# Kernel optimization log

Hardware: AMD Instinct MI355X
Metric: run time of the kernel (lower is better)

The kernel has to match this reference:

```python
import jax, jax.numpy as jnp
import numpy as np

B, U = 64, 512            # batch, max_units
AE = 1024
UE = 256                  # unit_embedding_size
A = 256                   # target_head_attention_size


def setup_inputs() -> dict:
    key = jax.random.key(0)
    ks = jax.random.split(key, 10)
    return {
        "autoregressive_embedding": jax.random.normal(ks[0], (B, U, AE), jnp.float32),
        "own_unit_embeddings": jax.random.normal(ks[1], (B, U, UE), jnp.float32),
        "enemy_unit_embeddings": jax.random.normal(ks[2], (B, U, UE), jnp.float32),
        "nr_own_units": jax.random.randint(ks[3], (B, 1), 0, U).astype(jnp.int64),
        "nr_units_enemy": jax.random.randint(ks[4], (B, 1), 0, U).astype(jnp.int64),
        "nr_own_flags": jax.random.randint(ks[5], (B, 1), 0, 8).astype(jnp.int64),
        "Wq": jax.random.normal(ks[6], (UE + AE, A), jnp.float32) * (1.0 / np.sqrt(UE + AE)),
        "bq": jnp.zeros((A,), jnp.float32),
        "Wk": jax.random.normal(ks[7], (UE, A), jnp.float32) * (1.0 / np.sqrt(UE)),
        "bk": jnp.zeros((A,), jnp.float32),
    }


def reference(autoregressive_embedding, own_unit_embeddings, enemy_unit_embeddings,
              nr_own_units, nr_units_enemy, nr_own_flags, Wq, bq, Wk, bk):
    # combined: [B, U, AE+UE]
    combined = jnp.concatenate([autoregressive_embedding, own_unit_embeddings], axis=2)
    queries = combined @ Wq + bq                       # [B, U, A]
    keys = enemy_unit_embeddings @ Wk + bk             # [B, U, A]
    attention = jnp.einsum("bqd,bkd->bqk", queries, keys) / (A ** 0.5)  # [B, U, U]
    # Vectorized mask: rows in [nr_own_flags, nr_own_units), cols in [0, nr_units_enemy)
    idx = jnp.arange(U)
    row_ok = (idx[None, :] >= nr_own_flags) & (idx[None, :] < nr_own_units)  # [B, U]
    col_ok = idx[None, :] < nr_units_enemy                                   # [B, U]
    mask = jnp.where(row_ok[:, :, None] & col_ok[:, None, :], 1.0, 1e-9)     # [B, U, U]
    return jax.nn.softmax(attention * mask, axis=-1)
```

## Files before the change

### kernel.cpp

```cpp
#include <hip/hip_runtime.h>

constexpr int B  = 64;
constexpr int U  = 512;
constexpr int AE = 1024;
constexpr int UE = 256;
constexpr int A  = 256;
constexpr int KQ = AE + UE;

typedef _Float16 f16x8 __attribute__((ext_vector_type(8)));
typedef float    f32x4 __attribute__((ext_vector_type(4)));

__global__ void prep(const float* __restrict__ Wq, const float* __restrict__ Wk,
                     _Float16* __restrict__ WqT, _Float16* __restrict__ WkT) {
    int idx = blockIdx.x * 256 + threadIdx.x;
    if (idx < KQ * A) {
        int k = idx >> 8, n = idx & 255;
        WqT[(size_t)n * KQ + k] = (_Float16)Wq[idx];
    } else {
        int j = idx - KQ * A;
        if (j < A * A) {
            int k = j >> 8, n = j & 255;
            WkT[(size_t)n * A + k] = (_Float16)Wk[j];
        }
    }
}

__global__ __launch_bounds__(256, 4) void gemm(
    const float* __restrict__ A1, int s1, int split,
    const float* __restrict__ A2, int s2,
    const _Float16* __restrict__ BT,
    const float* __restrict__ bias,
    _Float16* __restrict__ Out,
    int Ktot)
{
    __shared__ __align__(16) _Float16 Al[2][64][32];
    __shared__ __align__(16) _Float16 Bl[2][128][32];

    const int t    = threadIdx.x;
    const int lane = t & 63;
    const int w    = t >> 6;
    const int lm   = lane & 15;
    const int mbase = (blockIdx.x >> 1) * 64;
    const int nbase = (blockIdx.x & 1) * 128;

    const int wm  = (w & 1) * 32;
    const int wnl = (w >> 1) * 64;

    f32x4 acc[2][4] = {};

    const int ar = t & 63;
    const int kh = t >> 6;
    const int ap = kh >> 1;
    const size_t garow = mbase + ar;

    const int br = t >> 1;
    const int bs = t & 1;
    const size_t gbrow = nbase + br;

    float4 aR[4];
    f16x8  bR[4];

    auto loadA = [&](int k0) {
        int kg = k0 + kh * 16;
        const float* src = (kg < split) ? (A1 + garow * (size_t)s1 + kg)
                                        : (A2 + garow * (size_t)s2 + (kg - split));
        aR[0] = ((const float4*)src)[0];
        aR[1] = ((const float4*)src)[1];
        aR[2] = ((const float4*)src)[2];
        aR[3] = ((const float4*)src)[3];
    };
    auto loadB = [&](int k0) {
        const _Float16* src = BT + gbrow * (size_t)Ktot + k0 + bs * 32;
        bR[0] = ((const f16x8*)src)[0];
        bR[1] = ((const f16x8*)src)[1];
        bR[2] = ((const f16x8*)src)[2];
        bR[3] = ((const f16x8*)src)[3];
    };

    loadA(0);
    loadB(0);

    const int rsw = (lm >> 1) & 3;
    const int nk = Ktot >> 6;
    for (int kb = 0; kb < nk; kb++) {
        __syncthreads();
        {
            #pragma unroll
            for (int j = 0; j < 2; j++) {
                const float4 x = aR[j * 2], y = aR[j * 2 + 1];
                f16x8 hv;
                hv[0] = (_Float16)x.x; hv[1] = (_Float16)x.y;
                hv[2] = (_Float16)x.z; hv[3] = (_Float16)x.w;
                hv[4] = (_Float16)y.x; hv[5] = (_Float16)y.y;
                hv[6] = (_Float16)y.z; hv[7] = (_Float16)y.w;
                int c = (kh & 1) * 2 + j;
                *(f16x8*)(&Al[ap][ar][(c ^ ((ar >> 1) & 3)) * 8]) = hv;
            }
            #pragma unroll
            for (int j = 0; j < 4; j++)
                *(f16x8*)(&Bl[bs][br][(j ^ ((br >> 1) & 3)) * 8]) = bR[j];
        }
        __syncthreads();
        if (kb + 1 < nk) { loadA(kb * 64 + 64); loadB(kb * 64 + 64); }
        #pragma unroll
        for (int p = 0; p < 2; p++) {
            f16x8 af[2], bf[4];
            #pragma unroll
            for (int mt = 0; mt < 2; mt++)
                af[mt] = *(const f16x8*)(&Al[p][wm + mt * 16 + lm][((lane >> 4) ^ rsw) * 8]);
            #pragma unroll
            for (int nt = 0; nt < 4; nt++)
                bf[nt] = *(const f16x8*)(&Bl[p][wnl + nt * 16 + lm][((lane >> 4) ^ rsw) * 8]);
            #pragma unroll
            for (int mt = 0; mt < 2; mt++)
                #pragma unroll
                for (int nt = 0; nt < 4; nt++)
                    acc[mt][nt] = __builtin_amdgcn_mfma_f32_16x16x32_f16(
                        af[mt], bf[nt], acc[mt][nt], 0, 0, 0);
        }
    }

    const int rsub = (lane >> 4) * 4;
    #pragma unroll
    for (int nt = 0; nt < 4; nt++) {
        const int col = nbase + wnl + nt * 16 + lm;
        const float bv = bias[col];
        const int c5 = col >> 5, c31 = col & 31;
        #pragma unroll
        for (int mt = 0; mt < 2; mt++)
            #pragma unroll
            for (int r = 0; r < 4; r++) {
                int row = mbase + wm + mt * 16 + rsub + r;
                int bb = row >> 9, u = row & 511;
                Out[(((size_t)bb * 8 + c5) * 512 + u) * 32 + c31] =
                    (_Float16)(acc[mt][nt][r] + bv);
            }
    }
}

__global__ __launch_bounds__(256, 4) void attn(
    const _Float16* __restrict__ Qh, const _Float16* __restrict__ Kh,
    const int* __restrict__ nr_own_units, const int* __restrict__ nr_units_enemy,
    const int* __restrict__ nr_own_flags, float* __restrict__ Out)
{
    __shared__ float red[32][4];

    const int t    = threadIdx.x;
    const int lane = t & 63;
    const int w    = t >> 6;
    const int lm   = lane & 15;
    const int lk   = (lane >> 4) * 8;
    const int b    = blockIdx.y;
    const int qbase = blockIdx.x * 32;
    const int wn   = w * 128;

    const int nf = nr_own_flags[b];
    const int nu = nr_own_units[b];
    const int ne = nr_units_enemy[b];

    const _Float16* Qb = Qh + (size_t)b * 8 * 512 * 32;
    const _Float16* Kb = Kh + (size_t)b * 8 * 512 * 32;

    f32x4 acc[2][8] = {};

    #pragma unroll 2
    for (int c = 0; c < 8; c++) {
        f16x8 qf[2], bf[8];
        #pragma unroll
        for (int mt = 0; mt < 2; mt++)
            qf[mt] = *(const f16x8*)(Qb + ((size_t)c * 512 + qbase + mt * 16 + lm) * 32 + lk);
        #pragma unroll
        for (int nt = 0; nt < 8; nt++)
            bf[nt] = *(const f16x8*)(Kb + ((size_t)c * 512 + wn + nt * 16 + lm) * 32 + lk);
        #pragma unroll
        for (int mt = 0; mt < 2; mt++)
            #pragma unroll
            for (int nt = 0; nt < 8; nt++)
                acc[mt][nt] = __builtin_amdgcn_mfma_f32_16x16x32_f16(
                    qf[mt], bf[nt], acc[mt][nt], 0, 0, 0);
    }

    const int rsub = (lane >> 4) * 4;
    #pragma unroll
    for (int mt = 0; mt < 2; mt++)
        #pragma unroll
        for (int nt = 0; nt < 8; nt++)
            #pragma unroll
            for (int r = 0; r < 4; r++) {
                int uq = qbase + mt * 16 + rsub + r;
                int col = wn + nt * 16 + lm;
                bool ok = (col < ne) && (uq >= nf) && (uq < nu);
                acc[mt][nt][r] = acc[mt][nt][r] * 0.0625f * (ok ? 1.0f : 1e-9f);
            }

    float mx[2][4];
    #pragma unroll
    for (int mt = 0; mt < 2; mt++)
        #pragma unroll
        for (int r = 0; r < 4; r++) {
            float m = acc[mt][0][r];
            #pragma unroll
            for (int nt = 1; nt < 8; nt++) m = fmaxf(m, acc[mt][nt][r]);
            #pragma unroll
            for (int off = 1; off <= 8; off <<= 1) m = fmaxf(m, __shfl_xor(m, off));
            mx[mt][r] = m;
        }
    if (lm == 0) {
        #pragma unroll
        for (int mt = 0; mt < 2; mt++)
            #pragma unroll
            for (int r = 0; r < 4; r++)
                red[mt * 16 + rsub + r][w] = mx[mt][r];
    }
    __syncthreads();
    #pragma unroll
    for (int mt = 0; mt < 2; mt++)
        #pragma unroll
        for (int r = 0; r < 4; r++) {
            f32x4 v = *(const f32x4*)(&red[mt * 16 + rsub + r][0]);
            mx[mt][r] = fmaxf(fmaxf(v[0], v[1]), fmaxf(v[2], v[3]));
        }
    __syncthreads();

    float sm[2][4];
    #pragma unroll
    for (int mt = 0; mt < 2; mt++)
        #pragma unroll
        for (int r = 0; r < 4; r++) {
            float s = 0.f;
            #pragma unroll
            for (int nt = 0; nt < 8; nt++) {
                float e = __expf(acc[mt][nt][r] - mx[mt][r]);
                acc[mt][nt][r] = e;
                s += e;
            }
            #pragma unroll
            for (int off = 1; off <= 8; off <<= 1) s += __shfl_xor(s, off);
            sm[mt][r] = s;
        }
    if (lm == 0) {
        #pragma unroll
        for (int mt = 0; mt < 2; mt++)
            #pragma unroll
            for (int r = 0; r < 4; r++)
                red[mt * 16 + rsub + r][w] = sm[mt][r];
    }
    __syncthreads();

    #pragma unroll
    for (int mt = 0; mt < 2; mt++)
        #pragma unroll
        for (int r = 0; r < 4; r++) {
            int rl = mt * 16 + rsub + r;
            f32x4 v = *(const f32x4*)(&red[rl][0]);
            float inv = 1.0f / (v[0] + v[1] + v[2] + v[3]);
            float* orow = Out + ((size_t)b * 512 + qbase + rl) * 512 + wn + lm;
            #pragma unroll
            for (int nt = 0; nt < 8; nt++)
                orow[nt * 16] = acc[mt][nt][r] * inv;
        }
}

extern "C" void kernel_launch(void* const* d_in, const int* in_sizes, int n_in,
                              void* d_out, int out_size, void* d_ws, size_t ws_size,
                              hipStream_t stream) {
    const float* ar    = (const float*)d_in[0];
    const float* own   = (const float*)d_in[1];
    const float* enemy = (const float*)d_in[2];
    const int*   n_own   = (const int*)d_in[3];
    const int*   n_enemy = (const int*)d_in[4];
    const int*   n_flags = (const int*)d_in[5];
    const float* Wq = (const float*)d_in[6];
    const float* bq = (const float*)d_in[7];
    const float* Wk = (const float*)d_in[8];
    const float* bk = (const float*)d_in[9];
    float* out = (float*)d_out;

    char* ws = (char*)d_ws;
    _Float16* WqT = (_Float16*)(ws);
    _Float16* WkT = (_Float16*)(ws + 655360);
    _Float16* Qh  = (_Float16*)(ws + 786432);
    _Float16* Kh  = (_Float16*)(ws + 786432 + 16777216);

    prep<<<dim3((KQ * A + A * A) / 256), dim3(256), 0, stream>>>(Wq, Wk, WqT, WkT);

    gemm<<<dim3(1024), dim3(256), 0, stream>>>(ar, AE, AE, own, UE, WqT, bq, Qh, KQ);
    gemm<<<dim3(1024), dim3(256), 0, stream>>>(enemy, UE, 0, enemy, UE, WkT, bk, Kh, A);

    attn<<<dim3(16, B), dim3(256), 0, stream>>>(Qh, Kh, n_own, n_enemy, n_flags, out);
}
```

Baseline: 358.5 us.

## Enlarge GEMM tiles to full N width and stage Q/K through LDS in attention

The projection GEMM now uses 512-thread blocks covering 128 rows and all 256 output columns, so each fp32 activation row is read and converted once instead of twice. The attention kernel now processes 64 query rows per 512-thread block, stages the Q tile in LDS once and streams K chunks through swizzled LDS with register prefetch, instead of every wave loading fragments straight from global memory. This cuts redundant global traffic for the large fp32 input and for K. In exchange, blocks and register/LDS use per block grow, and the GEMM grid drops to 256 blocks, so occupancy and latency hiding may suffer.

Result: faster. 333.1 us (-7.1%).

```diff
diff --git a/kernel.cpp b/kernel.cpp
--- a/kernel.cpp
+++ b/kernel.cpp
@@ -25,7 +25,7 @@
     }
 }
 
-__global__ __launch_bounds__(256, 4) void gemm(
+__global__ __launch_bounds__(512, 1) void gemm(
     const float* __restrict__ A1, int s1, int split,
     const float* __restrict__ A2, int s2,
     const _Float16* __restrict__ BT,
@@ -33,35 +33,33 @@
     _Float16* __restrict__ Out,
     int Ktot)
 {
-    __shared__ __align__(16) _Float16 Al[2][64][32];
-    __shared__ __align__(16) _Float16 Bl[2][128][32];
+    __shared__ __align__(16) _Float16 Al[2][128][32];
+    __shared__ __align__(16) _Float16 Bl[2][256][32];
 
     const int t    = threadIdx.x;
     const int lane = t & 63;
     const int w    = t >> 6;
     const int lm   = lane & 15;
-    const int mbase = (blockIdx.x >> 1) * 64;
-    const int nbase = (blockIdx.x & 1) * 128;
-
-    const int wm  = (w & 1) * 32;
-    const int wnl = (w >> 1) * 64;
-
-    f32x4 acc[2][4] = {};
-
-    const int ar = t & 63;
-    const int kh = t >> 6;
-    const int ap = kh >> 1;
+    const int mbase = blockIdx.x * 128;
+
+    const int wm = (w & 1) * 64;
+    const int wn = (w >> 1) * 64;
+
+    f32x4 acc[4][4] = {};
+
+    const int ar = t >> 2;
+    const int as = t & 3;
+    const int ap = as >> 1;
     const size_t garow = mbase + ar;
 
     const int br = t >> 1;
     const int bs = t & 1;
-    const size_t gbrow = nbase + br;
 
     float4 aR[4];
     f16x8  bR[4];
 
     auto loadA = [&](int k0) {
-        int kg = k0 + kh * 16;
+        int kg = k0 + as * 16;
         const float* src = (kg < split) ? (A1 + garow * (size_t)s1 + kg)
                                         : (A2 + garow * (size_t)s2 + (kg - split));
         aR[0] = ((const float4*)src)[0];
@@ -70,7 +68,7 @@
         aR[3] = ((const float4*)src)[3];
     };
     auto loadB = [&](int k0) {
-        const _Float16* src = BT + gbrow * (size_t)Ktot + k0 + bs * 32;
+        const _Float16* src = BT + (size_t)br * Ktot + k0 + bs * 32;
         bR[0] = ((const f16x8*)src)[0];
         bR[1] = ((const f16x8*)src)[1];
         bR[2] = ((const f16x8*)src)[2];
@@ -93,7 +91,7 @@
                 hv[2] = (_Float16)x.z; hv[3] = (_Float16)x.w;
                 hv[4] = (_Float16)y.x; hv[5] = (_Float16)y.y;
                 hv[6] = (_Float16)y.z; hv[7] = (_Float16)y.w;
-                int c = (kh & 1) * 2 + j;
+                int c = (as & 1) * 2 + j;
                 *(f16x8*)(&Al[ap][ar][(c ^ ((ar >> 1) & 3)) * 8]) = hv;
             }
             #pragma unroll
@@ -104,15 +102,15 @@
         if (kb + 1 < nk) { loadA(kb * 64 + 64); loadB(kb * 64 + 64); }
         #pragma unroll
         for (int p = 0; p < 2; p++) {
-            f16x8 af[2], bf[4];
-            #pragma unroll
-            for (int mt = 0; mt < 2; mt++)
+            f16x8 af[4], bf[4];
+            #pragma unroll
+            for (int mt = 0; mt < 4; mt++)
                 af[mt] = *(const f16x8*)(&Al[p][wm + mt * 16 + lm][((lane >> 4) ^ rsw) * 8]);
             #pragma unroll
             for (int nt = 0; nt < 4; nt++)
-                bf[nt] = *(const f16x8*)(&Bl[p][wnl + nt * 16 + lm][((lane >> 4) ^ rsw) * 8]);
-            #pragma unroll
-            for (int mt = 0; mt < 2; mt++)
+                bf[nt] = *(const f16x8*)(&Bl[p][wn + nt * 16 + lm][((lane >> 4) ^ rsw) * 8]);
+            #pragma unroll
+            for (int mt = 0; mt < 4; mt++)
                 #pragma unroll
                 for (int nt = 0; nt < 4; nt++)
                     acc[mt][nt] = __builtin_amdgcn_mfma_f32_16x16x32_f16(
@@ -123,11 +121,11 @@
     const int rsub = (lane >> 4) * 4;
     #pragma unroll
     for (int nt = 0; nt < 4; nt++) {
-        const int col = nbase + wnl + nt * 16 + lm;
+        const int col = wn + nt * 16 + lm;
         const float bv = bias[col];
         const int c5 = col >> 5, c31 = col & 31;
         #pragma unroll
-        for (int mt = 0; mt < 2; mt++)
+        for (int mt = 0; mt < 4; mt++)
             #pragma unroll
             for (int r = 0; r < 4; r++) {
                 int row = mbase + wm + mt * 16 + rsub + r;
@@ -138,46 +136,78 @@
     }
 }
 
-__global__ __launch_bounds__(256, 4) void attn(
+__global__ __launch_bounds__(512, 2) void attn(
     const _Float16* __restrict__ Qh, const _Float16* __restrict__ Kh,
     const int* __restrict__ nr_own_units, const int* __restrict__ nr_units_enemy,
     const int* __restrict__ nr_own_flags, float* __restrict__ Out)
 {
-    __shared__ float red[32][4];
+    __shared__ __align__(16) _Float16 Ql[8][64][32];
+    __shared__ __align__(16) _Float16 Kl[512][32];
+    __shared__ float red[64][4];
 
     const int t    = threadIdx.x;
     const int lane = t & 63;
     const int w    = t >> 6;
     const int lm   = lane & 15;
-    const int lk   = (lane >> 4) * 8;
     const int b    = blockIdx.y;
-    const int qbase = blockIdx.x * 32;
-    const int wn   = w * 128;
+    const int qbase = blockIdx.x * 64;
+
+    const int wm = (w & 1) * 32;
+    const int wn = (w >> 1) * 128;
 
     const int nf = nr_own_flags[b];
     const int nu = nr_own_units[b];
     const int ne = nr_units_enemy[b];
 
-    const _Float16* Qb = Qh + (size_t)b * 8 * 512 * 32;
+    {
+        f16x8 qreg[4];
+        #pragma unroll
+        for (int j = 0; j < 4; j++) {
+            int s = j * 512 + t;
+            int p = s >> 8, row = (s & 255) >> 2, cq = s & 3;
+            qreg[j] = *(const f16x8*)(Qh + (((size_t)b * 8 + p) * 512 + qbase + row) * 32 + cq * 8);
+        }
+        #pragma unroll
+        for (int j = 0; j < 4; j++) {
+            int s = j * 512 + t;
+            int p = s >> 8, row = (s & 255) >> 2, cq = s & 3;
+            *(f16x8*)(&Ql[p][row][(cq ^ ((row >> 1) & 3)) * 8]) = qreg[j];
+        }
+    }
+
     const _Float16* Kb = Kh + (size_t)b * 8 * 512 * 32;
+    f16x8 kreg[4];
+    auto loadK = [&](int c) {
+        const _Float16* src = Kb + ((size_t)c * 512 + t) * 32;
+        kreg[0] = ((const f16x8*)src)[0];
+        kreg[1] = ((const f16x8*)src)[1];
+        kreg[2] = ((const f16x8*)src)[2];
+        kreg[3] = ((const f16x8*)src)[3];
+    };
+    loadK(0);
 
     f32x4 acc[2][8] = {};
-
-    #pragma unroll 2
+    const int rsw = (lm >> 1) & 3;
     for (int c = 0; c < 8; c++) {
-        f16x8 qf[2], bf[8];
+        __syncthreads();
+        #pragma unroll
+        for (int j = 0; j < 4; j++)
+            *(f16x8*)(&Kl[t][(j ^ ((t >> 1) & 3)) * 8]) = kreg[j];
+        __syncthreads();
+        if (c < 7) loadK(c + 1);
+        f16x8 af[2], bf[8];
         #pragma unroll
         for (int mt = 0; mt < 2; mt++)
-            qf[mt] = *(const f16x8*)(Qb + ((size_t)c * 512 + qbase + mt * 16 + lm) * 32 + lk);
+            af[mt] = *(const f16x8*)(&Ql[c][wm + mt * 16 + lm][((lane >> 4) ^ rsw) * 8]);
         #pragma unroll
         for (int nt = 0; nt < 8; nt++)
-            bf[nt] = *(const f16x8*)(Kb + ((size_t)c * 512 + wn + nt * 16 + lm) * 32 + lk);
+            bf[nt] = *(const f16x8*)(&Kl[wn + nt * 16 + lm][((lane >> 4) ^ rsw) * 8]);
         #pragma unroll
         for (int mt = 0; mt < 2; mt++)
             #pragma unroll
             for (int nt = 0; nt < 8; nt++)
                 acc[mt][nt] = __builtin_amdgcn_mfma_f32_16x16x32_f16(
-                    qf[mt], bf[nt], acc[mt][nt], 0, 0, 0);
+                    af[mt], bf[nt], acc[mt][nt], 0, 0, 0);
     }
 
     const int rsub = (lane >> 4) * 4;
@@ -187,7 +217,7 @@
         for (int nt = 0; nt < 8; nt++)
             #pragma unroll
             for (int r = 0; r < 4; r++) {
-                int uq = qbase + mt * 16 + rsub + r;
+                int uq = qbase + wm + mt * 16 + rsub + r;
                 int col = wn + nt * 16 + lm;
                 bool ok = (col < ne) && (uq >= nf) && (uq < nu);
                 acc[mt][nt][r] = acc[mt][nt][r] * 0.0625f * (ok ? 1.0f : 1e-9f);
@@ -210,14 +240,14 @@
         for (int mt = 0; mt < 2; mt++)
             #pragma unroll
             for (int r = 0; r < 4; r++)
-                red[mt * 16 + rsub + r][w] = mx[mt][r];
+                red[wm + mt * 16 + rsub + r][w >> 1] = mx[mt][r];
     }
     __syncthreads();
     #pragma unroll
     for (int mt = 0; mt < 2; mt++)
         #pragma unroll
         for (int r = 0; r < 4; r++) {
-            f32x4 v = *(const f32x4*)(&red[mt * 16 + rsub + r][0]);
+            f32x4 v = *(const f32x4*)(&red[wm + mt * 16 + rsub + r][0]);
             mx[mt][r] = fmaxf(fmaxf(v[0], v[1]), fmaxf(v[2], v[3]));
         }
     __syncthreads();
@@ -243,7 +273,7 @@
         for (int mt = 0; mt < 2; mt++)
             #pragma unroll
             for (int r = 0; r < 4; r++)
-                red[mt * 16 + rsub + r][w] = sm[mt][r];
+                red[wm + mt * 16 + rsub + r][w >> 1] = sm[mt][r];
     }
     __syncthreads();
 
@@ -251,7 +281,7 @@
     for (int mt = 0; mt < 2; mt++)
         #pragma unroll
         for (int r = 0; r < 4; r++) {
-            int rl = mt * 16 + rsub + r;
+            int rl = wm + mt * 16 + rsub + r;
             f32x4 v = *(const f32x4*)(&red[rl][0]);
             float inv = 1.0f / (v[0] + v[1] + v[2] + v[3]);
             float* orow = Out + ((size_t)b * 512 + qbase + rl) * 512 + wn + lm;
@@ -284,8 +314,8 @@
 
     prep<<<dim3((KQ * A + A * A) / 256), dim3(256), 0, stream>>>(Wq, Wk, WqT, WkT);
 
-    gemm<<<dim3(1024), dim3(256), 0, stream>>>(ar, AE, AE, own, UE, WqT, bq, Qh, KQ);
-    gemm<<<dim3(1024), dim3(256), 0, stream>>>(enemy, UE, 0, enemy, UE, WkT, bk, Kh, A);
-
-    attn<<<dim3(16, B), dim3(256), 0, stream>>>(Qh, Kh, n_own, n_enemy, n_flags, out);
+    gemm<<<dim3(256), dim3(512), 0, stream>>>(ar, AE, AE, own, UE, WqT, bq, Qh, KQ);
+    gemm<<<dim3(256), dim3(512), 0, stream>>>(enemy, UE, 0, enemy, UE, WkT, bk, Kh, A);
+
+    attn<<<dim3(8, B), dim3(512), 0, stream>>>(Qh, Kh, n_own, n_enemy, n_flags, out);
 }
```
